# Kernel tuning notes

Measured on AMD Instinct MI355X. Metric: run time of the kernel, lower is better.

## Reference

```python
import jax, jax.numpy as jnp
import numpy as np

KS = 3          # kernel_size
PAD = 1         # padding
STRIDE = 1      # stride
INC = 32
OUTC = 64
N = KS * KS     # number of sampling points


def conv2d(x, w, b, stride, pad):
    out = jax.lax.conv_general_dilated(
        x, w, (stride, stride), [(pad, pad), (pad, pad)],
        dimension_numbers=('NCHW', 'OIHW', 'NCHW'))
    return out if b is None else out + b[None, :, None, None]


def setup_inputs() -> dict:
    key = jax.random.key(0)
    k = jax.random.split(key, 5)
    x = jax.random.normal(k[0], (2, INC, 192, 192), jnp.float32)
    # main conv: kernel=ks, stride=ks, bias=None in the original
    conv_w = jax.random.normal(k[1], (OUTC, INC, KS, KS), jnp.float32) * (1.0 / np.sqrt(INC * KS * KS))
    # p_conv: weight init to 0 in the original (output = bias broadcast); unused in the math
    p_conv_w = jnp.zeros((2 * N, INC, 3, 3), jnp.float32)
    p_conv_b = jax.random.uniform(k[2], (2 * N,), jnp.float32, minval=-0.05, maxval=0.05)
    # p_conv1: produces scalar scale map A; keep it near 1 for realistic sampling
    p1_w = jax.random.normal(k[3], (1, INC, 3, 3), jnp.float32) * 0.05
    p1_b = jax.random.uniform(k[4], (1,), jnp.float32, minval=0.9, maxval=1.1)
    return {'x': x, 'conv_w': conv_w, 'p_conv_w': p_conv_w, 'p_conv_b': p_conv_b,
            'p1_w': p1_w, 'p1_b': p1_b}


def _gather_xq(xp, qx, qy, Wp):
    # xp: (b,c,Hp,Wp); qx,qy: (b,h,w,N) int -> (b,c,h,w,N)
    b, c = xp.shape[0], xp.shape[1]
    xf = xp.reshape(b, c, -1)
    idx = qx * Wp + qy  # linear index into flattened padded map (matches torch gather)
    def per_b(xf_b, idx_b):
        return xf_b[:, idx_b.ravel()].reshape((c,) + idx_b.shape)
    return jax.vmap(per_b)(xf, idx)


def _forward(x, conv_w, p_conv_w, p_conv_b, p1_w, p1_b):
    dt = x.dtype
    offset = conv2d(x, p_conv_w, p_conv_b, STRIDE, 1)   # (b,2N,h,w) -- shape-only in original
    A = conv2d(x, p1_w, p1_b, STRIDE, 1)                # (b,1,h,w) scale map
    h, w = offset.shape[2], offset.shape[3]
    xp = jnp.pad(x, ((0, 0), (0, 0), (PAD, PAD), (PAD, PAD)))
    Hp, Wp = xp.shape[2], xp.shape[3]

    # p_n: kernel-relative grid offsets, shape (1,2N,1,1)
    rng = jnp.arange(-(KS - 1) // 2, (KS - 1) // 2 + 1)
    pnx, pny = jnp.meshgrid(rng, rng, indexing='ij')
    p_n = jnp.concatenate([pnx.ravel(), pny.ravel()]).astype(dt).reshape(1, 2 * N, 1, 1)
    # p_0: absolute center coords starting at 1 (accounts for zero padding)
    gx, gy = jnp.meshgrid(jnp.arange(1, h * STRIDE + 1, STRIDE),
                          jnp.arange(1, w * STRIDE + 1, STRIDE), indexing='ij')
    p_0 = jnp.concatenate([jnp.tile(gx[None], (N, 1, 1)),
                           jnp.tile(gy[None], (N, 1, 1))], 0)[None].astype(dt)

    p = p_0 + A * p_n                       # (b,2N,h,w): scaled sampling grid
    p = jnp.transpose(p, (0, 2, 3, 1))      # (b,h,w,2N)

    q_lt = jnp.floor(p)
    q_rb = q_lt + 1
    qx_lt = jnp.clip(q_lt[..., :N], 0, Hp - 1).astype(jnp.int32)
    qy_lt = jnp.clip(q_lt[..., N:], 0, Wp - 1).astype(jnp.int32)
    qx_rb = jnp.clip(q_rb[..., :N], 0, Hp - 1).astype(jnp.int32)
    qy_rb = jnp.clip(q_rb[..., N:], 0, Wp - 1).astype(jnp.int32)

    px = jnp.clip(p[..., :N], 0, Hp - 1)
    py = jnp.clip(p[..., N:], 0, Wp - 1)

    fx_lt, fy_lt = qx_lt.astype(dt), qy_lt.astype(dt)
    fx_rb, fy_rb = qx_rb.astype(dt), qy_rb.astype(dt)
    g_lt = (1 + (fx_lt - px)) * (1 + (fy_lt - py))
    g_rb = (1 - (fx_rb - px)) * (1 - (fy_rb - py))
    g_lb = (1 + (fx_lt - px)) * (1 - (fy_rb - py))   # q_lb = (x_lt, y_rb)
    g_rt = (1 - (fx_rb - px)) * (1 + (fy_lt - py))   # q_rt = (x_rb, y_lt)

    x_lt = _gather_xq(xp, qx_lt, qy_lt, Wp)
    x_rb = _gather_xq(xp, qx_rb, qy_rb, Wp)
    x_lb = _gather_xq(xp, qx_lt, qy_rb, Wp)
    x_rt = _gather_xq(xp, qx_rb, qy_lt, Wp)

    # bilinear combine -> (b,c,h,w,N)
    x_offset = (g_lt[:, None] * x_lt + g_rb[:, None] * x_rb
                + g_lb[:, None] * x_lb + g_rt[:, None] * x_rt)

    # the ks-stride conv over the reshaped [h*ks, w*ks] map is exactly a
    # contraction over (c, n) with n = ki*ks + kj (same ordering as p_n flatten)
    wk = conv_w.reshape(conv_w.shape[0], conv_w.shape[1], N)
    out = jnp.einsum('ocn,bchwn->bohw', wk, x_offset)
    return out


def reference(x, conv_w, p_conv_w, p_conv_b, p1_w, p1_b):
    return _forward(x, conv_w, p_conv_w, p_conv_b, p1_w, p1_b)
```

## Files before the change

kernel.cpp:

```cpp
#include <hip/hip_runtime.h>

typedef __attribute__((ext_vector_type(4))) float f32x4;
typedef __attribute__((ext_vector_type(4))) int   i32x4;
typedef __attribute__((ext_vector_type(8))) short s16x8;

__device__ __forceinline__ unsigned short f2bf_rn(float f) {
  union { float f; unsigned u; } v; v.f = f;
  unsigned r = v.u + 0x7fffu + ((v.u >> 16) & 1u);
  return (unsigned short)(r >> 16);
}

__device__ __forceinline__ int packbf2(float lo, float hi) {
  union { float f; unsigned u; } a, b; a.f = lo; b.f = hi;
  return (int)__builtin_amdgcn_perm(b.u + 0x8000u, a.u + 0x8000u, 0x07060302u);
}

__device__ __forceinline__ void add8(i32x4 v, float g, f32x4& s0, f32x4& s1) {
  union { int ii; float ff; } u;
  u.ii = v[0] << 16;                  s0[0] = fmaf(g, u.ff, s0[0]);
  u.ii = v[0] & (int)0xffff0000u;     s0[1] = fmaf(g, u.ff, s0[1]);
  u.ii = v[1] << 16;                  s0[2] = fmaf(g, u.ff, s0[2]);
  u.ii = v[1] & (int)0xffff0000u;     s0[3] = fmaf(g, u.ff, s0[3]);
  u.ii = v[2] << 16;                  s1[0] = fmaf(g, u.ff, s1[0]);
  u.ii = v[2] & (int)0xffff0000u;     s1[1] = fmaf(g, u.ff, s1[1]);
  u.ii = v[3] << 16;                  s1[2] = fmaf(g, u.ff, s1[2]);
  u.ii = v[3] & (int)0xffff0000u;     s1[3] = fmaf(g, u.ff, s1[3]);
}

__device__ __forceinline__ void axis_cw(float p, int& il, int& ir, float& gl, float& gr) {
  float fl = floorf(p);
  float ql = fminf(fmaxf(fl, 0.f), 193.f);
  float qr = fminf(fmaxf(fl + 1.f, 0.f), 193.f);
  float pc = fminf(fmaxf(p, 0.f), 193.f);
  gl = 1.f + (ql - pc);
  gr = 1.f - (qr - pc);
  il = (int)ql; ir = (int)qr;
}

#define S_PAD (2 * 194 * 194 * 4)
#define S_WF  (9 * 4 * 64)
#define S_AM  (2 * 192 * 192 * 4)

__global__ __launch_bounds__(256) void k_prep(const float* __restrict__ x,
                                              unsigned short* __restrict__ xp,
                                              const float* __restrict__ w,
                                              short* __restrict__ wf,
                                              const float* __restrict__ p1w,
                                              const float* __restrict__ p1b,
                                              float* __restrict__ Amap) {
  int t = blockIdx.x * 256 + threadIdx.x;
  if (t < S_PAD) {
    int pix = t >> 2, c8 = t & 3;
    int b = pix / (194 * 194);
    int r = pix % (194 * 194);
    int i = r / 194 - 1, j = r % 194 - 1;
    bool ok = ((unsigned)i < 192u) && ((unsigned)j < 192u);
    const float* src = x + (size_t)b * 32 * 36864 + (size_t)(c8 * 8) * 36864 + i * 192 + j;
    unsigned v[8];
    #pragma unroll
    for (int k = 0; k < 8; k++) v[k] = ok ? (unsigned)f2bf_rn(src[k * 36864]) : 0u;
    i32x4 pv;
    pv[0] = (int)(v[0] | (v[1] << 16));
    pv[1] = (int)(v[2] | (v[3] << 16));
    pv[2] = (int)(v[4] | (v[5] << 16));
    pv[3] = (int)(v[6] | (v[7] << 16));
    *(i32x4*)(xp + (size_t)pix * 32 + c8 * 8) = pv;
  } else if (t < S_PAD + S_WF) {
    int u = t - S_PAD;
    int n = u / 256;
    int ot = (u / 64) % 4;
    int lane = u % 64;
    int o = ot * 16 + (lane & 15);
    int cb = (lane >> 4) * 8;
    #pragma unroll
    for (int jj = 0; jj < 8; jj++) {
      float v = w[(o * 32 + cb + jj) * 9 + n];
      wf[(size_t)u * 8 + jj] = (short)f2bf_rn(v);
    }
  } else {
    int u = t - S_PAD - S_WF;
    if (u >= S_AM) return;
    int pix = u >> 2, q = u & 3;
    int b = pix / 36864;
    int r = pix % 36864;
    int i = r / 192, j = r % 192;
    const float* xb = x + (size_t)b * 32 * 36864 + (size_t)(q * 8) * 36864;
    float a = 0.f;
    #pragma unroll
    for (int di = 0; di < 3; di++) {
      int ii = i + di - 1;
      bool rv = (unsigned)ii < 192u;
      #pragma unroll
      for (int dj = 0; dj < 3; dj++) {
        int jj = j + dj - 1;
        bool ok = rv && ((unsigned)jj < 192u);
        int tap = di * 3 + dj;
        #pragma unroll
        for (int k = 0; k < 8; k++) {
          float xv = ok ? xb[(size_t)k * 36864 + ii * 192 + jj] : 0.f;
          a = fmaf(xv, p1w[(q * 8 + k) * 9 + tap], a);
        }
      }
    }
    a += __shfl_xor(a, 1);
    a += __shfl_xor(a, 2);
    if (q == 0) Amap[pix] = a + p1b[0];
  }
}

__global__ __launch_bounds__(256, 4) void k_main(const unsigned short* __restrict__ xp,
                                                 const float* __restrict__ Amap,
                                                 const s16x8* __restrict__ wfv,
                                                 float* __restrict__ out) {
  int lane = threadIdx.x & 63;
  int bs = (blockIdx.x & 7) * 144 + (blockIdx.x >> 3);
  int W = bs * 4 + (threadIdx.x >> 6);
  int b = W / 2304;
  int r = W % 2304;
  int i = r / 12;
  int j0 = (r % 12) * 16;
  int m = lane & 15, quad = lane >> 4;
  int j = j0 + m;
  const unsigned short* xpb = xp + (size_t)b * (194 * 194 * 32) + quad * 8;
  float A = Amap[b * 36864 + i * 192 + j];

  float cx = (float)(i + 1), cy = (float)(j + 1);
  int icx = i + 1, icy = j + 1;

  int xlm, xrm, xlp, xrp, ylm, yrm, ylp, yrp;
  float gxlm, gxrm, gxlp, gxrp, gylm, gyrm, gylp, gyrp;
  axis_cw(cx - A, xlm, xrm, gxlm, gxrm);
  axis_cw(cx + A, xlp, xrp, gxlp, gxrp);
  axis_cw(cy - A, ylm, yrm, gylm, gyrm);
  axis_cw(cy + A, ylp, yrp, gylp, gyrp);

  int rT0 = xlm * 6208, rT1 = xrm * 6208;
  int rM  = icx * 6208;
  int rB0 = xlp * 6208, rB1 = xrp * 6208;
  int c0 = ylm * 32, c1 = yrm * 32, cC = icy * 32, c2 = ylp * 32, c3 = yrp * 32;

  i32x4 T00 = *(const i32x4*)(xpb + rT0 + c0);
  i32x4 T01 = *(const i32x4*)(xpb + rT0 + c1);
  i32x4 T0C = *(const i32x4*)(xpb + rT0 + cC);
  i32x4 T02 = *(const i32x4*)(xpb + rT0 + c2);
  i32x4 T03 = *(const i32x4*)(xpb + rT0 + c3);
  i32x4 T10 = *(const i32x4*)(xpb + rT1 + c0);
  i32x4 T11 = *(const i32x4*)(xpb + rT1 + c1);
  i32x4 T1C = *(const i32x4*)(xpb + rT1 + cC);
  i32x4 T12 = *(const i32x4*)(xpb + rT1 + c2);
  i32x4 T13 = *(const i32x4*)(xpb + rT1 + c3);
  i32x4 M0 = *(const i32x4*)(xpb + rM + c0);
  i32x4 M1 = *(const i32x4*)(xpb + rM + c1);
  i32x4 MC = *(const i32x4*)(xpb + rM + cC);
  i32x4 M2 = *(const i32x4*)(xpb + rM + c2);
  i32x4 M3 = *(const i32x4*)(xpb + rM + c3);

  f32x4 acc0 = {0.f, 0.f, 0.f, 0.f};
  f32x4 acc1 = acc0, acc2 = acc0, acc3 = acc0;

#define MFMA4(n, af)                                                              \
  { int wb = (n) * 256 + lane;                                                    \
    acc0 = __builtin_amdgcn_mfma_f32_16x16x32_bf16(af, wfv[wb],       acc0, 0, 0, 0); \
    acc1 = __builtin_amdgcn_mfma_f32_16x16x32_bf16(af, wfv[wb + 64],  acc1, 0, 0, 0); \
    acc2 = __builtin_amdgcn_mfma_f32_16x16x32_bf16(af, wfv[wb + 128], acc2, 0, 0, 0); \
    acc3 = __builtin_amdgcn_mfma_f32_16x16x32_bf16(af, wfv[wb + 192], acc3, 0, 0, 0); }

#define PROC4(n, dLT, dRB, dLB, dRT, gx_l, gx_r, gy_l, gy_r)                      \
  { f32x4 s0 = {0.f, 0.f, 0.f, 0.f}, s1 = s0;                                     \
    add8(dLT, (gx_l) * (gy_l), s0, s1);                                           \
    add8(dRB, (gx_r) * (gy_r), s0, s1);                                           \
    add8(dLB, (gx_l) * (gy_r), s0, s1);                                           \
    add8(dRT, (gx_r) * (gy_l), s0, s1);                                           \
    s16x8 af; int* ai = (int*)&af;                                                \
    ai[0] = packbf2(s0[0], s0[1]); ai[1] = packbf2(s0[2], s0[3]);                 \
    ai[2] = packbf2(s1[0], s1[1]); ai[3] = packbf2(s1[2], s1[3]);                 \
    MFMA4(n, af) }

#define PROC2(n, dL, dR, g_l, g_r)                                                \
  { f32x4 s0 = {0.f, 0.f, 0.f, 0.f}, s1 = s0;                                     \
    add8(dL, (g_l), s0, s1);                                                      \
    add8(dR, (g_r), s0, s1);                                                      \
    s16x8 af; int* ai = (int*)&af;                                                \
    ai[0] = packbf2(s0[0], s0[1]); ai[1] = packbf2(s0[2], s0[3]);                 \
    ai[2] = packbf2(s1[0], s1[1]); ai[3] = packbf2(s1[2], s1[3]);                 \
    MFMA4(n, af) }

  PROC4(0, T00, T11, T01, T10, gxlm, gxrm, gylm, gyrm)
  PROC2(1, T0C, T1C, gxlm, gxrm)
  PROC4(2, T02, T13, T03, T12, gxlm, gxrm, gylp, gyrp)

  i32x4 B00 = *(const i32x4*)(xpb + rB0 + c0);
  i32x4 B01 = *(const i32x4*)(xpb + rB0 + c1);
  i32x4 B0C = *(const i32x4*)(xpb + rB0 + cC);
  i32x4 B02 = *(const i32x4*)(xpb + rB0 + c2);
  i32x4 B03 = *(const i32x4*)(xpb + rB0 + c3);
  i32x4 B10 = *(const i32x4*)(xpb + rB1 + c0);
  i32x4 B11 = *(const i32x4*)(xpb + rB1 + c1);
  i32x4 B1C = *(const i32x4*)(xpb + rB1 + cC);
  i32x4 B12 = *(const i32x4*)(xpb + rB1 + c2);
  i32x4 B13 = *(const i32x4*)(xpb + rB1 + c3);

  PROC2(3, M0, M1, gylm, gyrm)
  {
    s16x8 af; int* ai = (int*)&af;
    ai[0] = MC[0]; ai[1] = MC[1]; ai[2] = MC[2]; ai[3] = MC[3];
    MFMA4(4, af)
  }
  PROC2(5, M2, M3, gylp, gyrp)

  PROC4(6, B00, B11, B01, B10, gxlp, gxrp, gylm, gyrm)
  PROC2(7, B0C, B1C, gxlp, gxrp)
  PROC4(8, B02, B13, B03, B12, gxlp, gxrp, gylp, gyrp)

#undef PROC4
#undef PROC2
#undef MFMA4

  int o0 = lane & 15;
  int jout = j0 + quad * 4;
  float* op = out + (size_t)b * 64 * 36864 + (size_t)o0 * 36864 + i * 192 + jout;
  *(f32x4*)(op) = acc0;
  *(f32x4*)(op + 16 * 36864) = acc1;
  *(f32x4*)(op + 32 * 36864) = acc2;
  *(f32x4*)(op + 48 * 36864) = acc3;
}

extern "C" void kernel_launch(void* const* d_in, const int* in_sizes, int n_in,
                              void* d_out, int out_size, void* d_ws, size_t ws_size,
                              hipStream_t stream) {
  const float* x      = (const float*)d_in[0];
  const float* conv_w = (const float*)d_in[1];
  const float* p1w    = (const float*)d_in[4];
  const float* p1b    = (const float*)d_in[5];
  float* out = (float*)d_out;

  unsigned short* xp = (unsigned short*)d_ws;
  short* wf   = (short*)(xp + 2 * 194 * 194 * 32);
  float* Amap = (float*)(wf + 9 * 256 * 8);

  int prep_threads = S_PAD + S_WF + S_AM;
  k_prep<<<(prep_threads + 255) / 256, 256, 0, stream>>>(x, xp, conv_w, wf, p1w, p1b, Amap);
  k_main<<<1152, 256, 0, stream>>>(xp, Amap, (const s16x8*)wf, out);
}
```

Before: 115.9 us.

## Fuse scale-map conv into main kernel and split taps across wave pairs

The p_conv1 scale map A was computed in the prep kernel from fp32 x and written to a global Amap. It is now computed inside the main kernel from the bf16 padded tensor, using LDS-staged weights and a cross-wave reduction. Each 16-pixel segment's nine sampling taps are also split across two waves, whose partial MFMA accumulators are summed through LDS before the store. This removes the Amap round trip and the heavy fp32 conv in the prep stage, and doubles the number of waves available for gather latency. In exchange it adds block barriers and LDS traffic, and A is now computed from bf16 inputs, which can slightly change precision.

```diff
diff --git a/kernel.cpp b/kernel.cpp
--- a/kernel.cpp
+++ b/kernel.cpp
@@ -39,15 +39,11 @@
 
 #define S_PAD (2 * 194 * 194 * 4)
 #define S_WF  (9 * 4 * 64)
-#define S_AM  (2 * 192 * 192 * 4)
 
 __global__ __launch_bounds__(256) void k_prep(const float* __restrict__ x,
                                               unsigned short* __restrict__ xp,
                                               const float* __restrict__ w,
-                                              short* __restrict__ wf,
-                                              const float* __restrict__ p1w,
-                                              const float* __restrict__ p1b,
-                                              float* __restrict__ Amap) {
+                                              short* __restrict__ wf) {
   int t = blockIdx.x * 256 + threadIdx.x;
   if (t < S_PAD) {
     int pix = t >> 2, c8 = t & 3;
@@ -65,8 +61,9 @@
     pv[2] = (int)(v[4] | (v[5] << 16));
     pv[3] = (int)(v[6] | (v[7] << 16));
     *(i32x4*)(xp + (size_t)pix * 32 + c8 * 8) = pv;
-  } else if (t < S_PAD + S_WF) {
+  } else {
     int u = t - S_PAD;
+    if (u >= S_WF) return;
     int n = u / 256;
     int ot = (u / 64) % 4;
     int lane = u % 64;
@@ -77,83 +74,74 @@
       float v = w[(o * 32 + cb + jj) * 9 + n];
       wf[(size_t)u * 8 + jj] = (short)f2bf_rn(v);
     }
-  } else {
-    int u = t - S_PAD - S_WF;
-    if (u >= S_AM) return;
-    int pix = u >> 2, q = u & 3;
-    int b = pix / 36864;
-    int r = pix % 36864;
-    int i = r / 192, j = r % 192;
-    const float* xb = x + (size_t)b * 32 * 36864 + (size_t)(q * 8) * 36864;
-    float a = 0.f;
-    #pragma unroll
-    for (int di = 0; di < 3; di++) {
-      int ii = i + di - 1;
-      bool rv = (unsigned)ii < 192u;
-      #pragma unroll
-      for (int dj = 0; dj < 3; dj++) {
-        int jj = j + dj - 1;
-        bool ok = rv && ((unsigned)jj < 192u);
-        int tap = di * 3 + dj;
-        #pragma unroll
-        for (int k = 0; k < 8; k++) {
-          float xv = ok ? xb[(size_t)k * 36864 + ii * 192 + jj] : 0.f;
-          a = fmaf(xv, p1w[(q * 8 + k) * 9 + tap], a);
-        }
-      }
-    }
-    a += __shfl_xor(a, 1);
-    a += __shfl_xor(a, 2);
-    if (q == 0) Amap[pix] = a + p1b[0];
   }
 }
 
 __global__ __launch_bounds__(256, 4) void k_main(const unsigned short* __restrict__ xp,
-                                                 const float* __restrict__ Amap,
+                                                 const float* __restrict__ p1w,
+                                                 const float* __restrict__ p1b,
                                                  const s16x8* __restrict__ wfv,
                                                  float* __restrict__ out) {
+  __shared__ float wlds[288];
+  __shared__ float redA[2][2][16];
+  __shared__ float redC[2][64][17];
+  for (int idx = threadIdx.x; idx < 288; idx += 256) {
+    int c = idx / 9, tap = idx % 9;
+    wlds[tap * 32 + c] = p1w[idx];
+  }
+  __syncthreads();
+
   int lane = threadIdx.x & 63;
-  int bs = (blockIdx.x & 7) * 144 + (blockIdx.x >> 3);
-  int W = bs * 4 + (threadIdx.x >> 6);
-  int b = W / 2304;
-  int r = W % 2304;
+  int wid  = threadIdx.x >> 6;
+  int pair = wid >> 1, half = wid & 1;
+  int bs = (blockIdx.x & 7) * 288 + (blockIdx.x >> 3);
+  int seg = bs * 2 + pair;
+  int b = seg / 2304;
+  int r = seg % 2304;
   int i = r / 12;
   int j0 = (r % 12) * 16;
   int m = lane & 15, quad = lane >> 4;
   int j = j0 + m;
   const unsigned short* xpb = xp + (size_t)b * (194 * 194 * 32) + quad * 8;
-  float A = Amap[b * 36864 + i * 192 + j];
+
+  float a0 = 0.f, a1 = 0.f, a2 = 0.f, a3 = 0.f;
+  i32x4 vcen = {0, 0, 0, 0};
+#define ATAP(tap)                                                              \
+  { i32x4 v = *(const i32x4*)(xpb + ((i + (tap) / 3) * 194 + (j + (tap) % 3)) * 32); \
+    if ((tap) == 4) vcen = v;                                                  \
+    const f32x4* wp = (const f32x4*)(wlds + (tap) * 32 + quad * 8);            \
+    f32x4 w0 = wp[0], w1 = wp[1];                                              \
+    union { int ii; float ff; } u;                                             \
+    u.ii = v[0] << 16;              a0 = fmaf(u.ff, w0[0], a0);                \
+    u.ii = v[0] & (int)0xffff0000u; a1 = fmaf(u.ff, w0[1], a1);                \
+    u.ii = v[1] << 16;              a2 = fmaf(u.ff, w0[2], a2);                \
+    u.ii = v[1] & (int)0xffff0000u; a3 = fmaf(u.ff, w0[3], a3);                \
+    u.ii = v[2] << 16;              a0 = fmaf(u.ff, w1[0], a0);                \
+    u.ii = v[2] & (int)0xffff0000u; a1 = fmaf(u.ff, w1[1], a1);                \
+    u.ii = v[3] << 16;              a2 = fmaf(u.ff, w1[2], a2);                \
+    u.ii = v[3] & (int)0xffff0000u; a3 = fmaf(u.ff, w1[3], a3); }
+  if (half == 0) {
+    ATAP(0) ATAP(1) ATAP(2) ATAP(3) ATAP(4)
+  } else {
+    ATAP(5) ATAP(6) ATAP(7) ATAP(8)
+  }
+#undef ATAP
+  float a = (a0 + a1) + (a2 + a3);
+  a += __shfl_xor(a, 16);
+  a += __shfl_xor(a, 32);
+  if (lane < 16) redA[pair][half][lane] = a;
+  __syncthreads();
+  float A = redA[pair][0][m] + redA[pair][1][m] + p1b[0];
 
   float cx = (float)(i + 1), cy = (float)(j + 1);
   int icx = i + 1, icy = j + 1;
-
-  int xlm, xrm, xlp, xrp, ylm, yrm, ylp, yrp;
-  float gxlm, gxrm, gxlp, gxrp, gylm, gyrm, gylp, gyrp;
-  axis_cw(cx - A, xlm, xrm, gxlm, gxrm);
-  axis_cw(cx + A, xlp, xrp, gxlp, gxrp);
+  int rM = icx * 6208;
+
+  int ylm, yrm, ylp, yrp;
+  float gylm, gyrm, gylp, gyrp;
   axis_cw(cy - A, ylm, yrm, gylm, gyrm);
   axis_cw(cy + A, ylp, yrp, gylp, gyrp);
-
-  int rT0 = xlm * 6208, rT1 = xrm * 6208;
-  int rM  = icx * 6208;
-  int rB0 = xlp * 6208, rB1 = xrp * 6208;
   int c0 = ylm * 32, c1 = yrm * 32, cC = icy * 32, c2 = ylp * 32, c3 = yrp * 32;
-
-  i32x4 T00 = *(const i32x4*)(xpb + rT0 + c0);
-  i32x4 T01 = *(const i32x4*)(xpb + rT0 + c1);
-  i32x4 T0C = *(const i32x4*)(xpb + rT0 + cC);
-  i32x4 T02 = *(const i32x4*)(xpb + rT0 + c2);
-  i32x4 T03 = *(const i32x4*)(xpb + rT0 + c3);
-  i32x4 T10 = *(const i32x4*)(xpb + rT1 + c0);
-  i32x4 T11 = *(const i32x4*)(xpb + rT1 + c1);
-  i32x4 T1C = *(const i32x4*)(xpb + rT1 + cC);
-  i32x4 T12 = *(const i32x4*)(xpb + rT1 + c2);
-  i32x4 T13 = *(const i32x4*)(xpb + rT1 + c3);
-  i32x4 M0 = *(const i32x4*)(xpb + rM + c0);
-  i32x4 M1 = *(const i32x4*)(xpb + rM + c1);
-  i32x4 MC = *(const i32x4*)(xpb + rM + cC);
-  i32x4 M2 = *(const i32x4*)(xpb + rM + c2);
-  i32x4 M3 = *(const i32x4*)(xpb + rM + c3);
 
   f32x4 acc0 = {0.f, 0.f, 0.f, 0.f};
   f32x4 acc1 = acc0, acc2 = acc0, acc3 = acc0;
@@ -185,44 +173,71 @@
     ai[2] = packbf2(s1[0], s1[1]); ai[3] = packbf2(s1[2], s1[3]);                 \
     MFMA4(n, af) }
 
-  PROC4(0, T00, T11, T01, T10, gxlm, gxrm, gylm, gyrm)
-  PROC2(1, T0C, T1C, gxlm, gxrm)
-  PROC4(2, T02, T13, T03, T12, gxlm, gxrm, gylp, gyrp)
-
-  i32x4 B00 = *(const i32x4*)(xpb + rB0 + c0);
-  i32x4 B01 = *(const i32x4*)(xpb + rB0 + c1);
-  i32x4 B0C = *(const i32x4*)(xpb + rB0 + cC);
-  i32x4 B02 = *(const i32x4*)(xpb + rB0 + c2);
-  i32x4 B03 = *(const i32x4*)(xpb + rB0 + c3);
-  i32x4 B10 = *(const i32x4*)(xpb + rB1 + c0);
-  i32x4 B11 = *(const i32x4*)(xpb + rB1 + c1);
-  i32x4 B1C = *(const i32x4*)(xpb + rB1 + cC);
-  i32x4 B12 = *(const i32x4*)(xpb + rB1 + c2);
-  i32x4 B13 = *(const i32x4*)(xpb + rB1 + c3);
-
-  PROC2(3, M0, M1, gylm, gyrm)
-  {
-    s16x8 af; int* ai = (int*)&af;
-    ai[0] = MC[0]; ai[1] = MC[1]; ai[2] = MC[2]; ai[3] = MC[3];
-    MFMA4(4, af)
-  }
-  PROC2(5, M2, M3, gylp, gyrp)
-
-  PROC4(6, B00, B11, B01, B10, gxlp, gxrp, gylm, gyrm)
-  PROC2(7, B0C, B1C, gxlp, gxrp)
-  PROC4(8, B02, B13, B03, B12, gxlp, gxrp, gylp, gyrp)
-
+  if (half == 0) {
+    int xlm, xrm; float gxlm, gxrm;
+    axis_cw(cx - A, xlm, xrm, gxlm, gxrm);
+    int rT0 = xlm * 6208, rT1 = xrm * 6208;
+    i32x4 T00 = *(const i32x4*)(xpb + rT0 + c0);
+    i32x4 T01 = *(const i32x4*)(xpb + rT0 + c1);
+    i32x4 T0C = *(const i32x4*)(xpb + rT0 + cC);
+    i32x4 T02 = *(const i32x4*)(xpb + rT0 + c2);
+    i32x4 T03 = *(const i32x4*)(xpb + rT0 + c3);
+    i32x4 T10 = *(const i32x4*)(xpb + rT1 + c0);
+    i32x4 T11 = *(const i32x4*)(xpb + rT1 + c1);
+    i32x4 T1C = *(const i32x4*)(xpb + rT1 + cC);
+    i32x4 T12 = *(const i32x4*)(xpb + rT1 + c2);
+    i32x4 T13 = *(const i32x4*)(xpb + rT1 + c3);
+    i32x4 M0  = *(const i32x4*)(xpb + rM + c0);
+    i32x4 M1  = *(const i32x4*)(xpb + rM + c1);
+    PROC4(0, T00, T11, T01, T10, gxlm, gxrm, gylm, gyrm)
+    PROC2(1, T0C, T1C, gxlm, gxrm)
+    PROC4(2, T02, T13, T03, T12, gxlm, gxrm, gylp, gyrp)
+    PROC2(3, M0, M1, gylm, gyrm)
+    { s16x8 af; int* ai = (int*)&af;
+      ai[0] = vcen[0]; ai[1] = vcen[1]; ai[2] = vcen[2]; ai[3] = vcen[3];
+      MFMA4(4, af) }
+  } else {
+    int xlp, xrp; float gxlp, gxrp;
+    axis_cw(cx + A, xlp, xrp, gxlp, gxrp);
+    int rB0 = xlp * 6208, rB1 = xrp * 6208;
+    i32x4 M2  = *(const i32x4*)(xpb + rM + c2);
+    i32x4 M3  = *(const i32x4*)(xpb + rM + c3);
+    i32x4 B00 = *(const i32x4*)(xpb + rB0 + c0);
+    i32x4 B01 = *(const i32x4*)(xpb + rB0 + c1);
+    i32x4 B0C = *(const i32x4*)(xpb + rB0 + cC);
+    i32x4 B02 = *(const i32x4*)(xpb + rB0 + c2);
+    i32x4 B03 = *(const i32x4*)(xpb + rB0 + c3);
+    i32x4 B10 = *(const i32x4*)(xpb + rB1 + c0);
+    i32x4 B11 = *(const i32x4*)(xpb + rB1 + c1);
+    i32x4 B1C = *(const i32x4*)(xpb + rB1 + cC);
+    i32x4 B12 = *(const i32x4*)(xpb + rB1 + c2);
+    i32x4 B13 = *(const i32x4*)(xpb + rB1 + c3);
+    PROC2(5, M2, M3, gylp, gyrp)
+    PROC4(6, B00, B11, B01, B10, gxlp, gxrp, gylm, gyrm)
+    PROC2(7, B0C, B1C, gxlp, gxrp)
+    PROC4(8, B02, B13, B03, B12, gxlp, gxrp, gylp, gyrp)
+  }
 #undef PROC4
 #undef PROC2
 #undef MFMA4
 
-  int o0 = lane & 15;
-  int jout = j0 + quad * 4;
-  float* op = out + (size_t)b * 64 * 36864 + (size_t)o0 * 36864 + i * 192 + jout;
-  *(f32x4*)(op) = acc0;
-  *(f32x4*)(op + 16 * 36864) = acc1;
-  *(f32x4*)(op + 32 * 36864) = acc2;
-  *(f32x4*)(op + 48 * 36864) = acc3;
+  if (half == 1) {
+    f32x4* dst = (f32x4*)&redC[pair][lane][0];
+    dst[0] = acc0; dst[1] = acc1; dst[2] = acc2; dst[3] = acc3;
+  }
+  __syncthreads();
+  if (half == 0) {
+    const float* src = &redC[pair][lane][0];
+    const f32x4* sv = (const f32x4*)src;
+    acc0 += sv[0]; acc1 += sv[1]; acc2 += sv[2]; acc3 += sv[3];
+    int o0 = lane & 15;
+    int jout = j0 + quad * 4;
+    float* op = out + (size_t)b * 64 * 36864 + (size_t)o0 * 36864 + i * 192 + jout;
+    *(f32x4*)(op) = acc0;
+    *(f32x4*)(op + 16 * 36864) = acc1;
+    *(f32x4*)(op + 32 * 36864) = acc2;
+    *(f32x4*)(op + 48 * 36864) = acc3;
+  }
 }
 
 extern "C" void kernel_launch(void* const* d_in, const int* in_sizes, int n_in,
@@ -235,10 +250,9 @@
   float* out = (float*)d_out;
 
   unsigned short* xp = (unsigned short*)d_ws;
-  short* wf   = (short*)(xp + 2 * 194 * 194 * 32);
-  float* Amap = (float*)(wf + 9 * 256 * 8);
-
-  int prep_threads = S_PAD + S_WF + S_AM;
-  k_prep<<<(prep_threads + 255) / 256, 256, 0, stream>>>(x, xp, conv_w, wf, p1w, p1b, Amap);
-  k_main<<<1152, 256, 0, stream>>>(xp, Amap, (const s16x8*)wf, out);
-}
+  short* wf = (short*)(xp + 2 * 194 * 194 * 32);
+
+  int prep_threads = S_PAD + S_WF;
+  k_prep<<<(prep_threads + 255) / 256, 256, 0, stream>>>(x, xp, conv_w, wf);
+  k_main<<<2304, 256, 0, stream>>>(xp, p1w, p1b, (const s16x8*)wf, out);
+}
```

Result: faster. 97.47 us (median of 2 runs) (-15.9%).

## Tile A-map conv through shared memory and software-pipeline gather loads

Applied to the files above, without the earlier changes.

The scale-map conv in the prep kernel now loads a 16x16 output tile plus halo for all 32 channels into LDS and computes each pixel from shared memory, instead of each thread reading 72 global values. The main kernel interleaves the gather loads with the bilinear/MFMA processing of earlier taps rather than loading 15 vectors up front, which lowers register pressure. Its launch bounds are raised to 5 waves per SIMD. The prep blocks now use about 41KB of LDS, which may limit occupancy of the padding blocks in the same kernel.

```diff
diff --git a/kernel.cpp b/kernel.cpp
--- a/kernel.cpp
+++ b/kernel.cpp
@@ -38,8 +38,9 @@
 }
 
 #define S_PAD (2 * 194 * 194 * 4)
-#define S_WF  (9 * 4 * 64)
-#define S_AM  (2 * 192 * 192 * 4)
+#define NPAD_BLK 1177
+#define NWF_BLK  9
+#define NAM_BLK  288
 
 __global__ __launch_bounds__(256) void k_prep(const float* __restrict__ x,
                                               unsigned short* __restrict__ xp,
@@ -48,8 +49,11 @@
                                               const float* __restrict__ p1w,
                                               const float* __restrict__ p1b,
                                               float* __restrict__ Amap) {
-  int t = blockIdx.x * 256 + threadIdx.x;
-  if (t < S_PAD) {
+  __shared__ float xt[32 * 324];
+  __shared__ float wl[288];
+  if (blockIdx.x < NPAD_BLK) {
+    int t = blockIdx.x * 256 + threadIdx.x;
+    if (t >= S_PAD) return;
     int pix = t >> 2, c8 = t & 3;
     int b = pix / (194 * 194);
     int r = pix % (194 * 194);
@@ -65,8 +69,9 @@
     pv[2] = (int)(v[4] | (v[5] << 16));
     pv[3] = (int)(v[6] | (v[7] << 16));
     *(i32x4*)(xp + (size_t)pix * 32 + c8 * 8) = pv;
-  } else if (t < S_PAD + S_WF) {
-    int u = t - S_PAD;
+  } else if (blockIdx.x < NPAD_BLK + NWF_BLK) {
+    int u = (blockIdx.x - NPAD_BLK) * 256 + threadIdx.x;
+    if (u >= 9 * 4 * 64) return;
     int n = u / 256;
     int ot = (u / 64) % 4;
     int lane = u % 64;
@@ -78,37 +83,41 @@
       wf[(size_t)u * 8 + jj] = (short)f2bf_rn(v);
     }
   } else {
-    int u = t - S_PAD - S_WF;
-    if (u >= S_AM) return;
-    int pix = u >> 2, q = u & 3;
-    int b = pix / 36864;
-    int r = pix % 36864;
-    int i = r / 192, j = r % 192;
-    const float* xb = x + (size_t)b * 32 * 36864 + (size_t)(q * 8) * 36864;
-    float a = 0.f;
+    int tid = blockIdx.x - (NPAD_BLK + NWF_BLK);
+    int b = tid / 144, rem = tid % 144;
+    int i0 = (rem / 12) * 16, j0 = (rem % 12) * 16;
+    for (int idx = threadIdx.x; idx < 288; idx += 256) wl[idx] = p1w[idx];
+    const float* xb = x + (size_t)b * 32 * 36864;
+    for (int idx = threadIdx.x; idx < 32 * 324; idx += 256) {
+      int c = idx / 324, rr = (idx % 324) / 18, cc = idx % 18;
+      int ii = i0 + rr - 1, jj = j0 + cc - 1;
+      float v = (((unsigned)ii < 192u) && ((unsigned)jj < 192u))
+                  ? xb[(size_t)c * 36864 + ii * 192 + jj] : 0.f;
+      xt[idx] = v;
+    }
+    __syncthreads();
+    int pr = threadIdx.x >> 4, pc = threadIdx.x & 15;
+    float a0 = 0.f, a1 = 0.f, a2 = 0.f, a3 = 0.f;
     #pragma unroll
-    for (int di = 0; di < 3; di++) {
-      int ii = i + di - 1;
-      bool rv = (unsigned)ii < 192u;
+    for (int c = 0; c < 32; c += 4) {
+      const float* b0 = xt + (c + 0) * 324;
+      const float* b1 = xt + (c + 1) * 324;
+      const float* b2 = xt + (c + 2) * 324;
+      const float* b3 = xt + (c + 3) * 324;
       #pragma unroll
-      for (int dj = 0; dj < 3; dj++) {
-        int jj = j + dj - 1;
-        bool ok = rv && ((unsigned)jj < 192u);
-        int tap = di * 3 + dj;
-        #pragma unroll
-        for (int k = 0; k < 8; k++) {
-          float xv = ok ? xb[(size_t)k * 36864 + ii * 192 + jj] : 0.f;
-          a = fmaf(xv, p1w[(q * 8 + k) * 9 + tap], a);
-        }
+      for (int tap = 0; tap < 9; tap++) {
+        int off = (pr + tap / 3) * 18 + pc + tap % 3;
+        a0 = fmaf(b0[off], wl[(c + 0) * 9 + tap], a0);
+        a1 = fmaf(b1[off], wl[(c + 1) * 9 + tap], a1);
+        a2 = fmaf(b2[off], wl[(c + 2) * 9 + tap], a2);
+        a3 = fmaf(b3[off], wl[(c + 3) * 9 + tap], a3);
       }
     }
-    a += __shfl_xor(a, 1);
-    a += __shfl_xor(a, 2);
-    if (q == 0) Amap[pix] = a + p1b[0];
+    Amap[b * 36864 + (i0 + pr) * 192 + j0 + pc] = (a0 + a1) + (a2 + a3) + p1b[0];
   }
 }
 
-__global__ __launch_bounds__(256, 4) void k_main(const unsigned short* __restrict__ xp,
+__global__ __launch_bounds__(256, 5) void k_main(const unsigned short* __restrict__ xp,
                                                  const float* __restrict__ Amap,
                                                  const s16x8* __restrict__ wfv,
                                                  float* __restrict__ out) {
@@ -139,22 +148,6 @@
   int rB0 = xlp * 6208, rB1 = xrp * 6208;
   int c0 = ylm * 32, c1 = yrm * 32, cC = icy * 32, c2 = ylp * 32, c3 = yrp * 32;
 
-  i32x4 T00 = *(const i32x4*)(xpb + rT0 + c0);
-  i32x4 T01 = *(const i32x4*)(xpb + rT0 + c1);
-  i32x4 T0C = *(const i32x4*)(xpb + rT0 + cC);
-  i32x4 T02 = *(const i32x4*)(xpb + rT0 + c2);
-  i32x4 T03 = *(const i32x4*)(xpb + rT0 + c3);
-  i32x4 T10 = *(const i32x4*)(xpb + rT1 + c0);
-  i32x4 T11 = *(const i32x4*)(xpb + rT1 + c1);
-  i32x4 T1C = *(const i32x4*)(xpb + rT1 + cC);
-  i32x4 T12 = *(const i32x4*)(xpb + rT1 + c2);
-  i32x4 T13 = *(const i32x4*)(xpb + rT1 + c3);
-  i32x4 M0 = *(const i32x4*)(xpb + rM + c0);
-  i32x4 M1 = *(const i32x4*)(xpb + rM + c1);
-  i32x4 MC = *(const i32x4*)(xpb + rM + cC);
-  i32x4 M2 = *(const i32x4*)(xpb + rM + c2);
-  i32x4 M3 = *(const i32x4*)(xpb + rM + c3);
-
   f32x4 acc0 = {0.f, 0.f, 0.f, 0.f};
   f32x4 acc1 = acc0, acc2 = acc0, acc3 = acc0;
 
@@ -165,55 +158,70 @@
     acc2 = __builtin_amdgcn_mfma_f32_16x16x32_bf16(af, wfv[wb + 128], acc2, 0, 0, 0); \
     acc3 = __builtin_amdgcn_mfma_f32_16x16x32_bf16(af, wfv[wb + 192], acc3, 0, 0, 0); }
 
-#define PROC4(n, dLT, dRB, dLB, dRT, gx_l, gx_r, gy_l, gy_r)                      \
-  { f32x4 s0 = {0.f, 0.f, 0.f, 0.f}, s1 = s0;                                     \
-    add8(dLT, (gx_l) * (gy_l), s0, s1);                                           \
-    add8(dRB, (gx_r) * (gy_r), s0, s1);                                           \
-    add8(dLB, (gx_l) * (gy_r), s0, s1);                                           \
-    add8(dRT, (gx_r) * (gy_l), s0, s1);                                           \
-    s16x8 af; int* ai = (int*)&af;                                                \
+#define LD4(n, rA, rB, cL, cR)                                                    \
+  i32x4 d##n##0 = *(const i32x4*)(xpb + (rA) + (cL));                             \
+  i32x4 d##n##1 = *(const i32x4*)(xpb + (rB) + (cR));                             \
+  i32x4 d##n##2 = *(const i32x4*)(xpb + (rA) + (cR));                             \
+  i32x4 d##n##3 = *(const i32x4*)(xpb + (rB) + (cL));
+#define LD2R(n, rA, rB, cc)                                                       \
+  i32x4 d##n##0 = *(const i32x4*)(xpb + (rA) + (cc));                             \
+  i32x4 d##n##1 = *(const i32x4*)(xpb + (rB) + (cc));
+#define LD2C(n, rr, cL, cR)                                                       \
+  i32x4 d##n##0 = *(const i32x4*)(xpb + (rr) + (cL));                             \
+  i32x4 d##n##1 = *(const i32x4*)(xpb + (rr) + (cR));
+#define LD1(n, rr, cc)                                                            \
+  i32x4 d##n##0 = *(const i32x4*)(xpb + (rr) + (cc));
+
+#define PACK_GO(n, s0, s1)                                                        \
+  { s16x8 af; int* ai = (int*)&af;                                                \
     ai[0] = packbf2(s0[0], s0[1]); ai[1] = packbf2(s0[2], s0[3]);                 \
     ai[2] = packbf2(s1[0], s1[1]); ai[3] = packbf2(s1[2], s1[3]);                 \
     MFMA4(n, af) }
 
-#define PROC2(n, dL, dR, g_l, g_r)                                                \
+#define P4(n, gxL, gxR, gyL, gyR)                                                 \
   { f32x4 s0 = {0.f, 0.f, 0.f, 0.f}, s1 = s0;                                     \
-    add8(dL, (g_l), s0, s1);                                                      \
-    add8(dR, (g_r), s0, s1);                                                      \
-    s16x8 af; int* ai = (int*)&af;                                                \
-    ai[0] = packbf2(s0[0], s0[1]); ai[1] = packbf2(s0[2], s0[3]);                 \
-    ai[2] = packbf2(s1[0], s1[1]); ai[3] = packbf2(s1[2], s1[3]);                 \
-    MFMA4(n, af) }
-
-  PROC4(0, T00, T11, T01, T10, gxlm, gxrm, gylm, gyrm)
-  PROC2(1, T0C, T1C, gxlm, gxrm)
-  PROC4(2, T02, T13, T03, T12, gxlm, gxrm, gylp, gyrp)
-
-  i32x4 B00 = *(const i32x4*)(xpb + rB0 + c0);
-  i32x4 B01 = *(const i32x4*)(xpb + rB0 + c1);
-  i32x4 B0C = *(const i32x4*)(xpb + rB0 + cC);
-  i32x4 B02 = *(const i32x4*)(xpb + rB0 + c2);
-  i32x4 B03 = *(const i32x4*)(xpb + rB0 + c3);
-  i32x4 B10 = *(const i32x4*)(xpb + rB1 + c0);
-  i32x4 B11 = *(const i32x4*)(xpb + rB1 + c1);
-  i32x4 B1C = *(const i32x4*)(xpb + rB1 + cC);
-  i32x4 B12 = *(const i32x4*)(xpb + rB1 + c2);
-  i32x4 B13 = *(const i32x4*)(xpb + rB1 + c3);
-
-  PROC2(3, M0, M1, gylm, gyrm)
+    add8(d##n##0, (gxL) * (gyL), s0, s1);                                         \
+    add8(d##n##1, (gxR) * (gyR), s0, s1);                                         \
+    add8(d##n##2, (gxL) * (gyR), s0, s1);                                         \
+    add8(d##n##3, (gxR) * (gyL), s0, s1);                                         \
+    PACK_GO(n, s0, s1) }
+
+#define P2(n, gL, gR)                                                             \
+  { f32x4 s0 = {0.f, 0.f, 0.f, 0.f}, s1 = s0;                                     \
+    add8(d##n##0, (gL), s0, s1);                                                  \
+    add8(d##n##1, (gR), s0, s1);                                                  \
+    PACK_GO(n, s0, s1) }
+
+  LD4(0, rT0, rT1, c0, c1)
+  LD2R(1, rT0, rT1, cC)
+  P4(0, gxlm, gxrm, gylm, gyrm)
+  LD4(2, rT0, rT1, c2, c3)
+  P2(1, gxlm, gxrm)
+  LD2C(3, rM, c0, c1)
+  P4(2, gxlm, gxrm, gylp, gyrp)
+  LD1(4, rM, cC)
+  P2(3, gylm, gyrm)
+  LD2C(5, rM, c2, c3)
   {
     s16x8 af; int* ai = (int*)&af;
-    ai[0] = MC[0]; ai[1] = MC[1]; ai[2] = MC[2]; ai[3] = MC[3];
+    ai[0] = d40[0]; ai[1] = d40[1]; ai[2] = d40[2]; ai[3] = d40[3];
     MFMA4(4, af)
   }
-  PROC2(5, M2, M3, gylp, gyrp)
-
-  PROC4(6, B00, B11, B01, B10, gxlp, gxrp, gylm, gyrm)
-  PROC2(7, B0C, B1C, gxlp, gxrp)
-  PROC4(8, B02, B13, B03, B12, gxlp, gxrp, gylp, gyrp)
-
-#undef PROC4
-#undef PROC2
+  LD4(6, rB0, rB1, c0, c1)
+  P2(5, gylp, gyrp)
+  LD2R(7, rB0, rB1, cC)
+  P4(6, gxlp, gxrp, gylm, gyrm)
+  LD4(8, rB0, rB1, c2, c3)
+  P2(7, gxlp, gxrp)
+  P4(8, gxlp, gxrp, gylp, gyrp)
+
+#undef LD4
+#undef LD2R
+#undef LD2C
+#undef LD1
+#undef P4
+#undef P2
+#undef PACK_GO
 #undef MFMA4
 
   int o0 = lane & 15;
@@ -238,7 +246,7 @@
   short* wf   = (short*)(xp + 2 * 194 * 194 * 32);
   float* Amap = (float*)(wf + 9 * 256 * 8);
 
-  int prep_threads = S_PAD + S_WF + S_AM;
-  k_prep<<<(prep_threads + 255) / 256, 256, 0, stream>>>(x, xp, conv_w, wf, p1w, p1b, Amap);
+  k_prep<<<NPAD_BLK + NWF_BLK + NAM_BLK, 256, 0, stream>>>(x, xp, conv_w, wf,
+                                                           p1w, p1b, Amap);
   k_main<<<1152, 256, 0, stream>>>(xp, Amap, (const s16x8*)wf, out);
 }
```

New measurement: 118.6 us. 1.02x slower.
